# Performance work log

Measured on AMD Instinct MI355X. Metric: run time of the kernel, lower is better.

Reference implementation:

```python
import jax, jax.numpy as jnp
import numpy as np

DIM = 512
HEADS = 8

def setup_inputs() -> dict:
    key = jax.random.key(0)
    ks = jax.random.split(key, 24)
    B, Nq, N3, N4, D = 8, 4096, 1024, 256, DIM
    def lin(k):
        k1, k2 = jax.random.split(k)
        s = 1.0 / np.sqrt(D)
        return (jax.random.uniform(k1, (D, D), jnp.float32, -s, s),
                jax.random.uniform(k2, (D,), jnp.float32, -s, s))
    Wq1, bq1 = lin(ks[0]); Wk1, bk1 = lin(ks[1]); Wv1, bv1 = lin(ks[2])
    Wq2, bq2 = lin(ks[3]); Wk2, bk2 = lin(ks[4]); Wv2, bv2 = lin(ks[5])
    sr = 1.0 / np.sqrt(2 * D)
    Wr = jax.random.uniform(ks[6], (D, 2 * D), jnp.float32, -sr, sr)
    br = jax.random.uniform(ks[7], (D,), jnp.float32, -sr, sr)
    return {
        'f2': jax.random.normal(ks[8], (B, Nq, D), jnp.float32),
        'f3': jax.random.normal(ks[9], (B, N3, D), jnp.float32),
        'f4': jax.random.normal(ks[10], (B, N4, D), jnp.float32),
        'f2_pos_embed': jax.random.normal(ks[11], (B, Nq, D), jnp.float32),
        'f3_pos_embed': jax.random.normal(ks[12], (B, N3, D), jnp.float32),
        'f4_pos_embed': jax.random.normal(ks[13], (B, N4, D), jnp.float32),
        'Wq1': Wq1, 'bq1': bq1, 'Wk1': Wk1, 'bk1': bk1, 'Wv1': Wv1, 'bv1': bv1,
        'Wq2': Wq2, 'bq2': bq2, 'Wk2': Wk2, 'bk2': bk2, 'Wv2': Wv2, 'bv2': bv2,
        'Wr': Wr, 'br': br,
    }

def _linear(x, W, b):
    return x @ W.T + b

def _efficient_branch(q, k, v, H):
    # q: [B,Nq,D], k/v: [B,Nk,D]. Split D into H heads of dh channels (contiguous).
    B, Nq, D = q.shape
    Nk = k.shape[1]
    dh = D // H
    q = q.reshape(B, Nq, H, dh)
    k = k.reshape(B, Nk, H, dh)
    v = v.reshape(B, Nk, H, dh)
    qs = jax.nn.softmax(q, axis=1)   # softmax over query positions (torch dim=2 in [B,C,N])
    ks = jax.nn.softmax(k, axis=3)   # softmax over head key channels (torch dim=1)
    # context[b,h,d,e] = sum_n ks[b,n,h,d] * v[b,n,h,e]  -> [B,H,dh,dh]
    context = jnp.einsum('bnhd,bnhe->bhde', ks, v)
    # attended[b,n,h,e] = sum_d context[b,h,d,e] * qs[b,n,h,d]
    attended = jnp.einsum('bhde,bnhd->bnhe', context, qs)
    return attended.reshape(B, Nq, D)

def reference(f2, f3, f4, f2_pos_embed, f3_pos_embed, f4_pos_embed,
              Wq1, bq1, Wk1, bk1, Wv1, bv1,
              Wq2, bq2, Wk2, bk2, Wv2, bv2, Wr, br):
    f2p = f2 + f2_pos_embed
    q1 = _linear(f2p, Wq1, bq1)
    q2 = _linear(f2p, Wq2, bq2)
    k3 = _linear(f3 + f3_pos_embed, Wk1, bk1)
    v3 = _linear(f3, Wv1, bv1)
    k4 = _linear(f4 + f4_pos_embed, Wk2, bk2)
    v4 = _linear(f4, Wv2, bv2)
    agg32 = _efficient_branch(q1, k3, v3, HEADS)  # [B,Nq,D]
    agg42 = _efficient_branch(q2, k4, v4, HEADS)  # [B,Nq,D]
    out = jnp.concatenate([agg32, agg42], axis=-1)
    return _linear(out, Wr, br)  # dropout p=0 -> identity
```

## Files before the change

### kernel.cpp

```cpp
#include <hip/hip_runtime.h>

typedef unsigned short ushort_t;
typedef unsigned int uint32;
typedef __attribute__((ext_vector_type(8))) short short8;
typedef __attribute__((ext_vector_type(4))) float f32x4;

static __device__ __forceinline__ ushort_t f2bf(float f) {
  uint32 u = __builtin_bit_cast(uint32, f);
  u += 0x7fffu + ((u >> 16) & 1u);
  return (ushort_t)(u >> 16);
}
static __device__ __forceinline__ float bf2f(ushort_t h) {
  return __builtin_bit_cast(float, (uint32)h << 16);
}

static __device__ __forceinline__ void gload_lds16(const ushort_t* g, ushort_t* l) {
  __builtin_amdgcn_global_load_lds(
      (const __attribute__((address_space(1))) uint32*)g,
      (__attribute__((address_space(3))) uint32*)l, 16, 0, 0);
}

static __device__ __forceinline__ ushort4 cvt4(float4 v) {
  ushort4 u;
  u.x = f2bf(v.x); u.y = f2bf(v.y); u.z = f2bf(v.z); u.w = f2bf(v.w);
  return u;
}
static __device__ __forceinline__ ushort4 cvt4s(float4 a, float4 b) {
  ushort4 u;
  u.x = f2bf(a.x + b.x); u.y = f2bf(a.y + b.y);
  u.z = f2bf(a.z + b.z); u.w = f2bf(a.w + b.w);
  return u;
}

static __device__ __forceinline__ void ctx_block(
    const ushort_t* __restrict__ ks3, const ushort_t* __restrict__ v3,
    const ushort_t* __restrict__ ks4, const ushort_t* __restrict__ v4,
    float* __restrict__ ctxP, int cb, ushort_t* sm) {
  ushort_t (*ks_s)[68] = reinterpret_cast<ushort_t(*)[68]>(sm);
  ushort_t (*v_s)[68] = reinterpret_cast<ushort_t(*)[68]>(sm + 4352);
  const int t = threadIdx.x;
  const ushort_t* ks; const ushort_t* v; float* dst; int Nk, bh, chunk;
  if (cb < 256) {
    bh = cb >> 2; chunk = cb & 3;
    ks = ks3; v = v3; Nk = 1024;
    dst = ctxP + (size_t)((bh << 2) + chunk) * 4096;
  } else {
    bh = cb - 256; chunk = 0;
    ks = ks4; v = v4; Nk = 256;
    dst = ctxP + 1048576 + (size_t)bh * 4096;
  }
  const int bb = bh >> 3, h = bh & 7;
  const int td = t & 15, te = t >> 4;
  float acc[4][4] = {};
  size_t rowBase = (size_t)bb * Nk + chunk * 256;
  for (int n0 = 0; n0 < 256; n0 += 64) {
#pragma unroll
    for (int i = 0; i < 4; i++) {
      int idx = i * 256 + t;
      int n = idx >> 4, dq = idx & 15;
      size_t g = (rowBase + n0 + n) * 512 + h * 64 + dq * 4;
      *reinterpret_cast<ushort4*>(&ks_s[n][dq * 4]) = *reinterpret_cast<const ushort4*>(ks + g);
      *reinterpret_cast<ushort4*>(&v_s[n][dq * 4]) = *reinterpret_cast<const ushort4*>(v + g);
    }
    __syncthreads();
#pragma unroll 8
    for (int n = 0; n < 64; n++) {
      ushort4 cu = *reinterpret_cast<const ushort4*>(&ks_s[n][td * 4]);
      ushort4 vu = *reinterpret_cast<const ushort4*>(&v_s[n][te * 4]);
      float ca[4] = {bf2f(cu.x), bf2f(cu.y), bf2f(cu.z), bf2f(cu.w)};
      float va[4] = {bf2f(vu.x), bf2f(vu.y), bf2f(vu.z), bf2f(vu.w)};
#pragma unroll
      for (int i = 0; i < 4; i++)
#pragma unroll
        for (int j = 0; j < 4; j++) acc[i][j] += ca[i] * va[j];
    }
    __syncthreads();
  }
#pragma unroll
  for (int i = 0; i < 4; i++) {
    float4 o = make_float4(acc[i][0], acc[i][1], acc[i][2], acc[i][3]);
    *reinterpret_cast<float4*>(&dst[(td * 4 + i) * 64 + te * 4]) = o;
  }
}

__global__ void prepA_kernel(const float* __restrict__ f3, const float* __restrict__ f3pe,
                             const float* __restrict__ f4, const float* __restrict__ f4pe,
                             const float* __restrict__ Wq1, const float* __restrict__ Wq2,
                             const float* __restrict__ Wk1, const float* __restrict__ Wv1,
                             const float* __restrict__ Wk2, const float* __restrict__ Wv2,
                             const float* __restrict__ bq1, const float* __restrict__ bq2,
                             ushort_t* __restrict__ f3p, ushort_t* __restrict__ f3b,
                             ushort_t* __restrict__ f4p, ushort_t* __restrict__ f4b,
                             ushort_t* __restrict__ WqB, ushort_t* __restrict__ Wk1B,
                             ushort_t* __restrict__ Wv1B, ushort_t* __restrict__ Wk2B,
                             ushort_t* __restrict__ Wv2B, float* __restrict__ bqc,
                             float* __restrict__ Z) {
  int b = blockIdx.x, t = threadIdx.x;
  if (b < 2048) {
    int i0 = b * 512 + t, i1 = i0 + 256;
    const float4* A4 = reinterpret_cast<const float4*>(f3);
    const float4* P4 = reinterpret_cast<const float4*>(f3pe);
    float4 a0 = A4[i0], a1 = A4[i1], p0 = P4[i0], p1 = P4[i1];
    reinterpret_cast<ushort4*>(f3b)[i0] = cvt4(a0);
    reinterpret_cast<ushort4*>(f3b)[i1] = cvt4(a1);
    reinterpret_cast<ushort4*>(f3p)[i0] = cvt4s(a0, p0);
    reinterpret_cast<ushort4*>(f3p)[i1] = cvt4s(a1, p1);
  } else if (b < 2560) {
    int i0 = (b - 2048) * 512 + t, i1 = i0 + 256;
    const float4* A4 = reinterpret_cast<const float4*>(f4);
    const float4* P4 = reinterpret_cast<const float4*>(f4pe);
    float4 a0 = A4[i0], a1 = A4[i1], p0 = P4[i0], p1 = P4[i1];
    reinterpret_cast<ushort4*>(f4b)[i0] = cvt4(a0);
    reinterpret_cast<ushort4*>(f4b)[i1] = cvt4(a1);
    reinterpret_cast<ushort4*>(f4p)[i0] = cvt4s(a0, p0);
    reinterpret_cast<ushort4*>(f4p)[i1] = cvt4s(a1, p1);
  } else if (b < 3328) {
    int u = b - 2560;
    int arr = u >> 7, i0 = (u & 127) * 512 + t, i1 = i0 + 256;
    const float* s; ushort_t* d;
    switch (arr) {
      case 0: s = Wq1; d = WqB; break;
      case 1: s = Wq2; d = WqB + 262144; break;
      case 2: s = Wk1; d = Wk1B; break;
      case 3: s = Wv1; d = Wv1B; break;
      case 4: s = Wk2; d = Wk2B; break;
      default: s = Wv2; d = Wv2B; break;
    }
    const float4* S4 = reinterpret_cast<const float4*>(s);
    float4 v0 = S4[i0], v1 = S4[i1];
    reinterpret_cast<ushort4*>(d)[i0] = cvt4(v0);
    reinterpret_cast<ushort4*>(d)[i1] = cvt4(v1);
  } else {
    for (int i = t; i < 512; i += 256) { bqc[i] = bq1[i]; bqc[512 + i] = bq2[i]; }
    for (int i = t; i < 8192; i += 256) Z[i] = 0.f;
  }
}

static __device__ __forceinline__ void gemm_core(
    const ushort_t* __restrict__ A, const ushort_t* __restrict__ Bt,
    int K, int mBase, int nBase, ushort_t* As, ushort_t* Bs, f32x4 acc[4][4]) {
  const int t = threadIdx.x;
  const int w = t >> 6, l = t & 63;
  const int l15 = l & 15, l4 = l >> 4;
  const int rowInSeg = l >> 3;
  const int srcOff = ((l & 7) ^ rowInSeg) << 3;
  const int wm = (w >> 1) * 64, wn = (w & 1) * 64;

  for (int k0 = 0; k0 < K; k0 += 64) {
#pragma unroll
    for (int i = 0; i < 4; i++) {
      int seg = w * 4 + i;
      int row = seg * 8 + rowInSeg;
      gload_lds16(A + (size_t)(mBase + row) * K + k0 + srcOff, As + seg * 512);
      gload_lds16(Bt + (size_t)(nBase + row) * K + k0 + srcOff, Bs + seg * 512);
    }
    __syncthreads();
#pragma unroll
    for (int kk = 0; kk < 2; kk++) {
      short8 af[4], bfr[4];
      const int kb = kk * 64 + l4 * 16;
#pragma unroll
      for (int f = 0; f < 4; f++) {
        int rowA = wm + f * 16 + l15;
        af[f] = *reinterpret_cast<const short8*>(
            reinterpret_cast<const char*>(As) + rowA * 128 + (kb ^ ((rowA & 7) << 4)));
        int rowB = wn + f * 16 + l15;
        bfr[f] = *reinterpret_cast<const short8*>(
            reinterpret_cast<const char*>(Bs) + rowB * 128 + (kb ^ ((rowB & 7) << 4)));
      }
#pragma unroll
      for (int fm = 0; fm < 4; fm++)
#pragma unroll
        for (int fn = 0; fn < 4; fn++)
          acc[fm][fn] = __builtin_amdgcn_mfma_f32_16x16x32_bf16(af[fm], bfr[fn], acc[fm][fn], 0, 0, 0);
    }
    __syncthreads();
  }
}

__global__ __launch_bounds__(256, 4)
void gemm_g1(const ushort_t* __restrict__ A, const ushort_t* __restrict__ Bt,
             const float* __restrict__ bias, ushort_t* __restrict__ E,
             float* __restrict__ Z,
             const ushort_t* __restrict__ ks3, const ushort_t* __restrict__ v3,
             const ushort_t* __restrict__ ks4, const ushort_t* __restrict__ v4,
             float* __restrict__ ctxP, int gemmBlocks) {
  __shared__ ushort_t smem[16384];
  if ((int)blockIdx.x >= gemmBlocks) {
    ctx_block(ks3, v3, ks4, v4, ctxP, blockIdx.x - gemmBlocks, smem);
    return;
  }
  ushort_t* As = smem;
  ushort_t* Bs = smem + 8192;
  const int bid = blockIdx.x;
  const int swz = (bid & 7) * 256 + (bid >> 3);
  const int mBase = (swz >> 3) * 128, nBase = (swz & 7) * 128;
  const int t = threadIdx.x, w = t >> 6, lane = t & 63;
  const int l15 = lane & 15, l4 = lane >> 4;
  const int wm = (w >> 1) * 64, wn = (w & 1) * 64;

  f32x4 acc[4][4];
#pragma unroll
  for (int i = 0; i < 4; i++)
#pragma unroll
    for (int j = 0; j < 4; j++) acc[i][j] = (f32x4){0.f, 0.f, 0.f, 0.f};

  gemm_core(A, Bt, 512, mBase, nBase, As, Bs, acc);

  const int N = 1024;
  float bcol[4], csum[4] = {0.f, 0.f, 0.f, 0.f};
#pragma unroll
  for (int fn = 0; fn < 4; fn++) bcol[fn] = bias[nBase + wn + fn * 16 + l15];
#pragma unroll
  for (int fm = 0; fm < 4; fm++) {
#pragma unroll
    for (int r = 0; r < 4; r++) {
      int row = mBase + wm + fm * 16 + l4 * 4 + r;
      float ex[4];
#pragma unroll
      for (int fn = 0; fn < 4; fn++) {
        ex[fn] = __expf(acc[fm][fn][r] + bcol[fn]);
        csum[fn] += ex[fn];
      }
#pragma unroll
      for (int fn = 0; fn < 4; fn++)
        E[(size_t)row * N + nBase + wn + fn * 16 + l15] = f2bf(ex[fn]);
    }
  }
#pragma unroll
  for (int fn = 0; fn < 4; fn++) {
    float s = csum[fn];
    s += __shfl_xor(s, 16);
    s += __shfl_xor(s, 32);
    if (l4 == 0) atomicAdd(&Z[(mBase >> 12) * 1024 + nBase + wn + fn * 16 + l15], s);
  }
}

__global__ __launch_bounds__(256, 4)
void kv_quad(const ushort_t* __restrict__ f3p, const ushort_t* __restrict__ f3b,
             const ushort_t* __restrict__ f4p, const ushort_t* __restrict__ f4b,
             const ushort_t* __restrict__ Wk1B, const ushort_t* __restrict__ Wv1B,
             const ushort_t* __restrict__ Wk2B, const ushort_t* __restrict__ Wv2B,
             const float* __restrict__ bk1, const float* __restrict__ bv1,
             const float* __restrict__ bk2, const float* __restrict__ bv2,
             ushort_t* __restrict__ ks3, ushort_t* __restrict__ v3,
             ushort_t* __restrict__ ks4, ushort_t* __restrict__ v4,
             const float* __restrict__ f2, const float* __restrict__ f2pe,
             ushort_t* __restrict__ f2p) {
  __shared__ ushort_t As[8192], Bs[8192];
  const int bid = blockIdx.x;
  if (bid >= 640) {
    const int base = (bid - 640) * 2048;
    const float4* A4 = reinterpret_cast<const float4*>(f2);
    const float4* P4 = reinterpret_cast<const float4*>(f2pe);
    const int t = threadIdx.x;
#pragma unroll
    for (int half = 0; half < 2; half++) {
      float4 a[4], p[4];
#pragma unroll
      for (int j = 0; j < 4; j++) {
        int i = base + (half * 4 + j) * 256 + t;
        a[j] = A4[i];
        p[j] = P4[i];
      }
#pragma unroll
      for (int j = 0; j < 4; j++) {
        int i = base + (half * 4 + j) * 256 + t;
        reinterpret_cast<ushort4*>(f2p)[i] = cvt4s(a[j], p[j]);
      }
    }
    return;
  }
  const int id = (bid & 7) * 80 + (bid >> 3);
  const ushort_t* A; const ushort_t* Bt; const float* bias; ushort_t* out;
  bool doSM; int loc;
  if (id < 256)      { A = f3p; Bt = Wk1B; bias = bk1; out = ks3; doSM = true;  loc = id; }
  else if (id < 512) { A = f3b; Bt = Wv1B; bias = bv1; out = v3;  doSM = false; loc = id - 256; }
  else if (id < 576) { A = f4p; Bt = Wk2B; bias = bk2; out = ks4; doSM = true;  loc = id - 512; }
  else               { A = f4b; Bt = Wv2B; bias = bv2; out = v4;  doSM = false; loc = id - 576; }
  const int nBase = (loc & 3) * 128, mBase = (loc >> 2) * 128;
  const int t = threadIdx.x, w = t >> 6, lane = t & 63;
  const int l15 = lane & 15, l4 = lane >> 4;
  const int wm = (w >> 1) * 64, wn = (w & 1) * 64;

  f32x4 acc[4][4];
#pragma unroll
  for (int i = 0; i < 4; i++)
#pragma unroll
    for (int j = 0; j < 4; j++) acc[i][j] = (f32x4){0.f, 0.f, 0.f, 0.f};

  gemm_core(A, Bt, 512, mBase, nBase, As, Bs, acc);

  const int N = 512;
  float bcol[4];
#pragma unroll
  for (int fn = 0; fn < 4; fn++) bcol[fn] = bias[nBase + wn + fn * 16 + l15];

  if (doSM) {
#pragma unroll
    for (int fm = 0; fm < 4; fm++) {
#pragma unroll
      for (int r = 0; r < 4; r++) {
        float x[4], m = -1e30f;
#pragma unroll
        for (int fn = 0; fn < 4; fn++) { x[fn] = acc[fm][fn][r] + bcol[fn]; m = fmaxf(m, x[fn]); }
        m = fmaxf(m, __shfl_xor(m, 1));
        m = fmaxf(m, __shfl_xor(m, 2));
        m = fmaxf(m, __shfl_xor(m, 4));
        m = fmaxf(m, __shfl_xor(m, 8));
        float s = 0.f;
#pragma unroll
        for (int fn = 0; fn < 4; fn++) { x[fn] = __expf(x[fn] - m); s += x[fn]; }
        s += __shfl_xor(s, 1);
        s += __shfl_xor(s, 2);
        s += __shfl_xor(s, 4);
        s += __shfl_xor(s, 8);
        float inv = 1.f / s;
        int row = mBase + wm + fm * 16 + l4 * 4 + r;
#pragma unroll
        for (int fn = 0; fn < 4; fn++)
          out[(size_t)row * N + nBase + wn + fn * 16 + l15] = f2bf(x[fn] * inv);
      }
    }
  } else {
#pragma unroll
    for (int fm = 0; fm < 4; fm++) {
#pragma unroll
      for (int r = 0; r < 4; r++) {
        int row = mBase + wm + fm * 16 + l4 * 4 + r;
#pragma unroll
        for (int fn = 0; fn < 4; fn++)
          out[(size_t)row * N + nBase + wn + fn * 16 + l15] =
              f2bf(acc[fm][fn][r] + bcol[fn]);
      }
    }
  }
}

__global__ __launch_bounds__(256)
void ctxprepB_kernel(const ushort_t* __restrict__ ks3, const ushort_t* __restrict__ v3,
                     const ushort_t* __restrict__ ks4, const ushort_t* __restrict__ v4,
                     float* __restrict__ ctxP,
                     const float* __restrict__ f2, const float* __restrict__ f2pe,
                     ushort_t* __restrict__ f2p) {
  __shared__ ushort_t sm[8704];
  const int b = blockIdx.x, t = threadIdx.x;
  if (b >= 320) {
    const int base = (b - 320) * 1024;
    const float4* A4 = reinterpret_cast<const float4*>(f2);
    const float4* P4 = reinterpret_cast<const float4*>(f2pe);
#pragma unroll
    for (int j = 0; j < 4; j++) {
      int i = base + j * 256 + t;
      float4 a = A4[i], p = P4[i];
      reinterpret_cast<ushort4*>(f2p)[i] = cvt4s(a, p);
    }
    return;
  }
  ctx_block(ks3, v3, ks4, v4, ctxP, b, sm);
}

__global__ __launch_bounds__(256, 4)
void gemm_g2(const ushort_t* __restrict__ E, const ushort_t* __restrict__ Mt,
             const float* __restrict__ bias, float* __restrict__ C) {
  __shared__ ushort_t As[8192], Bs[8192];
  const int bid = blockIdx.x;
  const int swz = (bid & 7) * 128 + (bid >> 3);
  const int tx = swz & 3, ty = swz >> 2;
  const int mBase = ty * 128, nBase = tx * 128;
  const ushort_t* Btb = Mt + (size_t)(ty >> 5) * 524288;
  const int t = threadIdx.x, w = t >> 6, lane = t & 63;
  const int l15 = lane & 15, l4 = lane >> 4;
  const int wm = (w >> 1) * 64, wn = (w & 1) * 64;

  f32x4 acc[4][4];
#pragma unroll
  for (int i = 0; i < 4; i++)
#pragma unroll
    for (int j = 0; j < 4; j++) acc[i][j] = (f32x4){0.f, 0.f, 0.f, 0.f};

  gemm_core(E, Btb, 1024, mBase, nBase, As, Bs, acc);

  const int N = 512;
  float bcol[4];
#pragma unroll
  for (int fn = 0; fn < 4; fn++) bcol[fn] = bias[nBase + wn + fn * 16 + l15];
#pragma unroll
  for (int fm = 0; fm < 4; fm++) {
#pragma unroll
    for (int r = 0; r < 4; r++) {
      int row = mBase + wm + fm * 16 + l4 * 4 + r;
#pragma unroll
      for (int fn = 0; fn < 4; fn++)
        C[(size_t)row * N + nBase + wn + fn * 16 + l15] = acc[fm][fn][r] + bcol[fn];
    }
  }
}

__global__ __launch_bounds__(256)
void fold_kernel(const float* __restrict__ ctxP, const float* __restrict__ Wr,
                 const float* __restrict__ Z, ushort_t* __restrict__ Mt) {
  __shared__ float ctxT[64][68];
  __shared__ float wrT[64][68];
  __shared__ float zinv[64];
  int blk = blockIdx.x;
  int jc = blk & 7;
  int h = (blk >> 3) & 7;
  int branch = (blk >> 6) & 1;
  int b = blk >> 7;
  int t = threadIdx.x;
  int cbase = branch * 512 + h * 64;
  if (branch == 0) {
    const float* p = ctxP + (size_t)((b * 8 + h) * 4) * 4096;
#pragma unroll
    for (int i = 0; i < 16; i++) {
      int idx = i * 256 + t;
      int d = idx >> 6, e = idx & 63;
      int o = d * 64 + e;
      ctxT[e][d] = p[o] + p[4096 + o] + p[8192 + o] + p[12288 + o];
    }
  } else {
    const float* p = ctxP + 1048576 + (size_t)(b * 8 + h) * 4096;
#pragma unroll
    for (int i = 0; i < 16; i++) {
      int idx = i * 256 + t;
      int d = idx >> 6, e = idx & 63;
      ctxT[e][d] = p[d * 64 + e];
    }
  }
#pragma unroll
  for (int i = 0; i < 16; i++) {
    int idx = i * 256 + t;
    int jl = idx >> 6, e = idx & 63;
    wrT[e][jl] = Wr[(size_t)(jc * 64 + jl) * 1024 + cbase + e];
  }
  if (t < 64) zinv[t] = 1.0f / Z[b * 1024 + cbase + t];
  __syncthreads();
  int td = t & 15, tj = t >> 4;
  float acc[4][4] = {};
#pragma unroll 8
  for (int e = 0; e < 64; e++) {
    float4 cv = *reinterpret_cast<const float4*>(&ctxT[e][td * 4]);
    float4 wv = *reinterpret_cast<const float4*>(&wrT[e][tj * 4]);
    float ca[4] = {cv.x, cv.y, cv.z, cv.w};
    float wa[4] = {wv.x, wv.y, wv.z, wv.w};
#pragma unroll
    for (int i = 0; i < 4; i++)
#pragma unroll
      for (int jj = 0; jj < 4; jj++) acc[i][jj] += ca[i] * wa[jj];
  }
  float zi[4] = {zinv[td * 4], zinv[td * 4 + 1], zinv[td * 4 + 2], zinv[td * 4 + 3]};
#pragma unroll
  for (int jj = 0; jj < 4; jj++) {
    ushort4 u;
    u.x = f2bf(acc[0][jj] * zi[0]);
    u.y = f2bf(acc[1][jj] * zi[1]);
    u.z = f2bf(acc[2][jj] * zi[2]);
    u.w = f2bf(acc[3][jj] * zi[3]);
    *reinterpret_cast<ushort4*>(
        &Mt[(size_t)(b * 512 + jc * 64 + tj * 4 + jj) * 1024 + cbase + td * 4]) = u;
  }
}

extern "C" void kernel_launch(void* const* d_in, const int* in_sizes, int n_in,
                              void* d_out, int out_size, void* d_ws, size_t ws_size,
                              hipStream_t stream) {
  const float* f2 = (const float*)d_in[0];
  const float* f3 = (const float*)d_in[1];
  const float* f4 = (const float*)d_in[2];
  const float* f2pe = (const float*)d_in[3];
  const float* f3pe = (const float*)d_in[4];
  const float* f4pe = (const float*)d_in[5];
  const float* Wq1 = (const float*)d_in[6];
  const float* bq1 = (const float*)d_in[7];
  const float* Wk1 = (const float*)d_in[8];
  const float* bk1 = (const float*)d_in[9];
  const float* Wv1 = (const float*)d_in[10];
  const float* bv1 = (const float*)d_in[11];
  const float* Wq2 = (const float*)d_in[12];
  const float* bq2 = (const float*)d_in[13];
  const float* Wk2 = (const float*)d_in[14];
  const float* bk2 = (const float*)d_in[15];
  const float* Wv2 = (const float*)d_in[16];
  const float* bv2 = (const float*)d_in[17];
  const float* Wr = (const float*)d_in[18];
  const float* br = (const float*)d_in[19];

  char* ws = (char*)d_ws;
  ushort_t* E = (ushort_t*)(ws + 0);
  char* R1 = ws + 67108864;
  ushort_t* f3p = (ushort_t*)R1;
  ushort_t* f3b = (ushort_t*)(R1 + 8388608);
  ushort_t* f4p = (ushort_t*)(R1 + 16777216);
  ushort_t* f4b = (ushort_t*)(R1 + 18874368);
  char* R2 = ws + 100663296;
  ushort_t* ks3 = (ushort_t*)R2;
  ushort_t* v3b = (ushort_t*)(R2 + 8388608);
  ushort_t* ks4 = (ushort_t*)(R2 + 16777216);
  ushort_t* v4b = (ushort_t*)(R2 + 18874368);
  char* R3 = ws + 121634816;
  ushort_t* WqB = (ushort_t*)R3;
  ushort_t* Wk1B = (ushort_t*)(R3 + 1048576);
  ushort_t* Wv1B = (ushort_t*)(R3 + 1572864);
  ushort_t* Wk2B = (ushort_t*)(R3 + 2097152);
  ushort_t* Wv2B = (ushort_t*)(R3 + 2621440);
  ushort_t* Mt = (ushort_t*)(R3 + 3145728);
  float* Z = (float*)(R3 + 11534336);
  float* bqc = (float*)(R3 + 11567104);
  float* ctxP = (float*)(R3 + 11571200);
  const bool bigWS = ws_size >= (size_t)176160768;
  ushort_t* f2p = bigWS ? (ushort_t*)(ws + 142606336) : (ushort_t*)R1;

  prepA_kernel<<<3329, 256, 0, stream>>>(f3, f3pe, f4, f4pe,
                                         Wq1, Wq2, Wk1, Wv1, Wk2, Wv2, bq1, bq2,
                                         f3p, f3b, f4p, f4b,
                                         WqB, Wk1B, Wv1B, Wk2B, Wv2B, bqc, Z);

  if (bigWS) {
    kv_quad<<<2688, 256, 0, stream>>>(f3p, f3b, f4p, f4b,
                                      Wk1B, Wv1B, Wk2B, Wv2B,
                                      bk1, bv1, bk2, bv2,
                                      ks3, v3b, ks4, v4b, f2, f2pe, f2p);
    gemm_g1<<<2368, 256, 0, stream>>>(f2p, WqB, bqc, E, Z,
                                      ks3, v3b, ks4, v4b, ctxP, 2048);
  } else {
    kv_quad<<<640, 256, 0, stream>>>(f3p, f3b, f4p, f4b,
                                     Wk1B, Wv1B, Wk2B, Wv2B,
                                     bk1, bv1, bk2, bv2,
                                     ks3, v3b, ks4, v4b, f2, f2pe, f2p);
    ctxprepB_kernel<<<4416, 256, 0, stream>>>(ks3, v3b, ks4, v4b, ctxP, f2, f2pe, f2p);
    gemm_g1<<<2048, 256, 0, stream>>>(f2p, WqB, bqc, E, Z,
                                      ks3, v3b, ks4, v4b, ctxP, 2048);
  }

  fold_kernel<<<1024, 256, 0, stream>>>(ctxP, Wr, Z, Mt);

  gemm_g2<<<1024, 256, 0, stream>>>(E, Mt, br, (float*)d_out);
}
```

Before: 177.8 us.

## Split context computation out of gemm_g1 and raise occupancy bounds to 5

Moves the context-accumulation work out of gemm_g1 (where it ran as extra blocks) into a separate ctx_kernel launched before the GEMM. The f2 pos-embed prep becomes its own prepB_kernel in the small-workspace path. The launch bounds of gemm_g1, kv_quad and gemm_g2 go from 4 to 5 waves per SIMD, which caps register use. The aim is simpler GEMM kernels with higher occupancy, at the cost of an extra kernel launch and the lost overlap between the ctx blocks and the GEMM tiles. The tighter register cap may also cause spills.

Result: slower. 315.9 us (+77.7%).

```diff
diff --git a/kernel.cpp b/kernel.cpp
--- a/kernel.cpp
+++ b/kernel.cpp
@@ -32,13 +32,14 @@
   return u;
 }
 
-static __device__ __forceinline__ void ctx_block(
-    const ushort_t* __restrict__ ks3, const ushort_t* __restrict__ v3,
-    const ushort_t* __restrict__ ks4, const ushort_t* __restrict__ v4,
-    float* __restrict__ ctxP, int cb, ushort_t* sm) {
+__global__ __launch_bounds__(256)
+void ctx_kernel(const ushort_t* __restrict__ ks3, const ushort_t* __restrict__ v3,
+                const ushort_t* __restrict__ ks4, const ushort_t* __restrict__ v4,
+                float* __restrict__ ctxP) {
+  __shared__ ushort_t sm[8704];
   ushort_t (*ks_s)[68] = reinterpret_cast<ushort_t(*)[68]>(sm);
   ushort_t (*v_s)[68] = reinterpret_cast<ushort_t(*)[68]>(sm + 4352);
-  const int t = threadIdx.x;
+  const int cb = blockIdx.x, t = threadIdx.x;
   const ushort_t* ks; const ushort_t* v; float* dst; int Nk, bh, chunk;
   if (cb < 256) {
     bh = cb >> 2; chunk = cb & 3;
@@ -178,20 +179,11 @@
   }
 }
 
-__global__ __launch_bounds__(256, 4)
+__global__ __launch_bounds__(256, 5)
 void gemm_g1(const ushort_t* __restrict__ A, const ushort_t* __restrict__ Bt,
              const float* __restrict__ bias, ushort_t* __restrict__ E,
-             float* __restrict__ Z,
-             const ushort_t* __restrict__ ks3, const ushort_t* __restrict__ v3,
-             const ushort_t* __restrict__ ks4, const ushort_t* __restrict__ v4,
-             float* __restrict__ ctxP, int gemmBlocks) {
-  __shared__ ushort_t smem[16384];
-  if ((int)blockIdx.x >= gemmBlocks) {
-    ctx_block(ks3, v3, ks4, v4, ctxP, blockIdx.x - gemmBlocks, smem);
-    return;
-  }
-  ushort_t* As = smem;
-  ushort_t* Bs = smem + 8192;
+             float* __restrict__ Z) {
+  __shared__ ushort_t As[8192], Bs[8192];
   const int bid = blockIdx.x;
   const int swz = (bid & 7) * 256 + (bid >> 3);
   const int mBase = (swz >> 3) * 128, nBase = (swz & 7) * 128;
@@ -236,7 +228,7 @@
   }
 }
 
-__global__ __launch_bounds__(256, 4)
+__global__ __launch_bounds__(256, 5)
 void kv_quad(const ushort_t* __restrict__ f3p, const ushort_t* __restrict__ f3b,
              const ushort_t* __restrict__ f4p, const ushort_t* __restrict__ f4b,
              const ushort_t* __restrict__ Wk1B, const ushort_t* __restrict__ Wv1B,
@@ -338,29 +330,20 @@
 }
 
 __global__ __launch_bounds__(256)
-void ctxprepB_kernel(const ushort_t* __restrict__ ks3, const ushort_t* __restrict__ v3,
-                     const ushort_t* __restrict__ ks4, const ushort_t* __restrict__ v4,
-                     float* __restrict__ ctxP,
-                     const float* __restrict__ f2, const float* __restrict__ f2pe,
-                     ushort_t* __restrict__ f2p) {
-  __shared__ ushort_t sm[8704];
-  const int b = blockIdx.x, t = threadIdx.x;
-  if (b >= 320) {
-    const int base = (b - 320) * 1024;
-    const float4* A4 = reinterpret_cast<const float4*>(f2);
-    const float4* P4 = reinterpret_cast<const float4*>(f2pe);
-#pragma unroll
-    for (int j = 0; j < 4; j++) {
-      int i = base + j * 256 + t;
-      float4 a = A4[i], p = P4[i];
-      reinterpret_cast<ushort4*>(f2p)[i] = cvt4s(a, p);
-    }
-    return;
-  }
-  ctx_block(ks3, v3, ks4, v4, ctxP, b, sm);
-}
-
-__global__ __launch_bounds__(256, 4)
+void prepB_kernel(const float* __restrict__ f2, const float* __restrict__ f2pe,
+                  ushort_t* __restrict__ f2p) {
+  const int base = blockIdx.x * 1024, t = threadIdx.x;
+  const float4* A4 = reinterpret_cast<const float4*>(f2);
+  const float4* P4 = reinterpret_cast<const float4*>(f2pe);
+#pragma unroll
+  for (int j = 0; j < 4; j++) {
+    int i = base + j * 256 + t;
+    float4 a = A4[i], p = P4[i];
+    reinterpret_cast<ushort4*>(f2p)[i] = cvt4s(a, p);
+  }
+}
+
+__global__ __launch_bounds__(256, 5)
 void gemm_g2(const ushort_t* __restrict__ E, const ushort_t* __restrict__ Mt,
              const float* __restrict__ bias, float* __restrict__ C) {
   __shared__ ushort_t As[8192], Bs[8192];
@@ -521,17 +504,17 @@
                                       Wk1B, Wv1B, Wk2B, Wv2B,
                                       bk1, bv1, bk2, bv2,
                                       ks3, v3b, ks4, v4b, f2, f2pe, f2p);
-    gemm_g1<<<2368, 256, 0, stream>>>(f2p, WqB, bqc, E, Z,
-                                      ks3, v3b, ks4, v4b, ctxP, 2048);
   } else {
     kv_quad<<<640, 256, 0, stream>>>(f3p, f3b, f4p, f4b,
                                      Wk1B, Wv1B, Wk2B, Wv2B,
                                      bk1, bv1, bk2, bv2,
                                      ks3, v3b, ks4, v4b, f2, f2pe, f2p);
-    ctxprepB_kernel<<<4416, 256, 0, stream>>>(ks3, v3b, ks4, v4b, ctxP, f2, f2pe, f2p);
-    gemm_g1<<<2048, 256, 0, stream>>>(f2p, WqB, bqc, E, Z,
-                                      ks3, v3b, ks4, v4b, ctxP, 2048);
-  }
+    prepB_kernel<<<4096, 256, 0, stream>>>(f2, f2pe, f2p);
+  }
+
+  ctx_kernel<<<320, 256, 0, stream>>>(ks3, v3b, ks4, v4b, ctxP);
+
+  gemm_g1<<<2048, 256, 0, stream>>>(f2p, WqB, bqc, E, Z);
 
   fold_kernel<<<1024, 256, 0, stream>>>(ctxP, Wr, Z, Mt);
 
```
